# Optimization experiments

Measured on AMD Instinct MI355X. Metric: run time of the kernel, lower is better.

The kernel has to match this reference:

```python
import jax, jax.numpy as jnp
import numpy as np

B, C, H, W = 256, 3, 84, 84
HID, VOCAB = 768, 50257
INPUT_DIM = H * W
EPS = 1e-8


def setup_inputs() -> dict:
    key = jax.random.key(0)
    k1, k2, k3 = jax.random.split(key, 3)
    observations = jax.random.normal(k1, (B, C, H, W), dtype=jnp.float32)
    word_embs = jax.random.normal(k2, (VOCAB, HID), dtype=jnp.float32)
    # torch.normal(mean=0, std=1/sqrt(hidden_dim), size=(hidden_dim, input_dim))
    rand_obs_proj = jax.random.normal(k3, (HID, INPUT_DIM), dtype=jnp.float32) / np.sqrt(HID)
    return {"observations": observations, "word_embs": word_embs,
            "rand_obs_proj": rand_obs_proj, "beta": 8}


def reference(observations, word_embs, rand_obs_proj, beta):
    # _preprocess_obs: mean over channel dim, then flatten each sample
    obs = observations.mean(axis=1).reshape(observations.shape[0], -1)  # [B, H*W]
    q = obs @ rand_obs_proj.T                                           # [B, HID]
    q_norm = jnp.linalg.norm(q, axis=-1, keepdims=True)                 # [B, 1]
    e_norm = jnp.linalg.norm(word_embs, axis=-1)[None, :]               # [1, V]
    sims = (q @ word_embs.T) / (q_norm * e_norm + EPS)                  # [B, V]
    softm = jax.nn.softmax(beta * sims, axis=-1)
    state = softm @ word_embs                                           # [B, HID]
    return state
```

## Files before the change

### kernel.cpp

```cpp
#include <hip/hip_runtime.h>


#define VOCAB 50257
#define VPAD  50304
#define HID   768
#define BATCH 256
#define IN    7056
#define INPAD 7072
#define NPAIR (INPAD / 2)
#define SPLITS 32
#define CHUNK 1600
#define QSPLITS 17
#define QCHUNK 416

typedef __attribute__((ext_vector_type(8))) __bf16 bf16x8;
typedef __attribute__((ext_vector_type(4))) float f32x4;

__device__ inline unsigned short f2bf(float f) {
  union { float f; unsigned u; } v; v.f = f;
  unsigned r = v.u + 0x7fffu + ((v.u >> 16) & 1u);
  return (unsigned short)(r >> 16);
}
__device__ inline unsigned pack2(float lo, float hi) {
  return (unsigned)f2bf(lo) | ((unsigned)f2bf(hi) << 16);
}

__global__ __launch_bounds__(256, 3) void k_wprep(const float* __restrict__ W,
                                                  unsigned* __restrict__ Wb,
                                                  unsigned* __restrict__ WbT,
                                                  float* __restrict__ inv_en) {
  __shared__ unsigned short Sb[32][772];
  __shared__ float ssb[32][8];
  const int t = threadIdx.x;
  const int lane = t & 63, wave = t >> 6;
  const int v0 = blockIdx.x * 32;

  float4 xv[8][3];
#pragma unroll
  for (int rr = 0; rr < 8; rr++) {
    const int v = v0 + wave * 8 + rr;
    const int vc = (v < VOCAB) ? v : (VOCAB - 1);
    const float* wrow = &W[(size_t)vc * HID + lane * 4];
#pragma unroll
    for (int c = 0; c < 3; c++)
      xv[rr][c] = *(const float4*)(wrow + c * 256);
  }
#pragma unroll
  for (int rr = 0; rr < 8; rr++) {
    const int row = wave * 8 + rr;
    const int v = v0 + row;
    const bool valid = (v < VOCAB);
    unsigned* wbrow = &Wb[(size_t)v * (HID / 2) + lane * 2];
    float ss = 0.f;
#pragma unroll
    for (int c = 0; c < 3; c++) {
      float4 x = xv[rr][c];
      if (!valid) x = (float4){0.f, 0.f, 0.f, 0.f};
      unsigned lo = pack2(x.x, x.y), hi = pack2(x.z, x.w);
      *(uint2*)&Sb[row][c * 256 + lane * 4] = (uint2){lo, hi};
      *(uint2*)&wbrow[c * 128] = (uint2){lo, hi};
      ss += x.x * x.x + x.y * x.y + x.z * x.z + x.w * x.w;
    }
    ss += __shfl_xor(ss, 1, 64);
    ss += __shfl_xor(ss, 2, 64);
    ss += __shfl_xor(ss, 4, 64);
    if ((lane & 7) == 0) ssb[row][lane >> 3] = ss;
  }
  __syncthreads();
  {
    const int row = t >> 3, j = t & 7;
    float s = ssb[row][j];
    s += __shfl_xor(s, 1, 64);
    s += __shfl_xor(s, 2, 64);
    s += __shfl_xor(s, 4, 64);
    if (j == 0) {
      const int v = v0 + row;
      inv_en[v] = (v < VOCAB) ? (1.f / sqrtf(s)) : 0.f;
    }
  }
  for (int p = 0; p < 12; p++) {
    int hr = p * 64 + (t >> 2), li = t & 3;
    unsigned u[4];
    for (int j = 0; j < 4; j++) {
      int vl = li * 8 + j * 2;
      u[j] = (unsigned)Sb[vl][hr] | ((unsigned)Sb[vl + 1][hr] << 16);
    }
    *(uint4*)&WbT[(size_t)hr * (VPAD / 2) + (v0 >> 1) + li * 4] = *(const uint4*)u;
  }
}

__global__ __launch_bounds__(256) void k_obs(const float* __restrict__ obs,
                                             unsigned* __restrict__ obsb) {
  int b = blockIdx.x, t = threadIdx.x;
  const size_t base = (size_t)b * 3 * IN;
  for (int p = t; p < NPAIR; p += 256) {
    float x = 0.f, y = 0.f;
    if (2 * p < IN) {
      float2 a0 = *(const float2*)&obs[base + 2 * p];
      float2 a1 = *(const float2*)&obs[base + IN + 2 * p];
      float2 a2 = *(const float2*)&obs[base + 2 * IN + 2 * p];
      x = (a0.x + a1.x + a2.x) * (1.f / 3.f);
      y = (a0.y + a1.y + a2.y) * (1.f / 3.f);
    }
    obsb[b * NPAIR + p] = pack2(x, y);
  }
}

__global__ __launch_bounds__(256) void k_proj(const float* __restrict__ proj,
                                              unsigned* __restrict__ projb) {
  int h = blockIdx.x, t = threadIdx.x;
  for (int p = t; p < NPAIR; p += 256) {
    float x = 0.f, y = 0.f;
    if (2 * p < IN) {
      float2 xy = *(const float2*)&proj[(size_t)h * IN + 2 * p];
      x = xy.x; y = xy.y;
    }
    projb[h * NPAIR + p] = pack2(x, y);
  }
}


__global__ __launch_bounds__(256) void k_qgemm(const unsigned short* __restrict__ A,
                                               const unsigned short* __restrict__ Bm,
                                               float* __restrict__ qp) {
  __shared__ unsigned short As[64][32];
  __shared__ unsigned short Bs[64][32];
  const int t = threadIdx.x;
  const int lane = t & 63, wave = t >> 6;
  const int wm = wave >> 1, wn = wave & 1;
  const int quad = lane >> 4, lo = lane & 15;
  const int m0 = blockIdx.y * 64, n0 = blockIdx.x * 64;
  const int split = blockIdx.z;
  const int kbeg = split * QCHUNK, kend = kbeg + QCHUNK;
  const int ar = t >> 2, ac = (t & 3) * 8;
  f32x4 acc[2][2];
  for (int i = 0; i < 2; i++)
    for (int j = 0; j < 2; j++) acc[i][j] = (f32x4){0.f, 0.f, 0.f, 0.f};
  const unsigned short* aptr = &A[(m0 + ar) * INPAD + ac];
  const unsigned short* bptr = &Bm[(n0 + ar) * INPAD + ac];
  for (int k0 = kbeg; k0 < kend; k0 += 32) {
    uint4 av = *(const uint4*)(aptr + k0);
    uint4 bv = *(const uint4*)(bptr + k0);
    __syncthreads();
    *(uint4*)&As[ar][ac] = av;
    *(uint4*)&Bs[ar][ac] = bv;
    __syncthreads();
    bf16x8 af[2], bfr[2];
    for (int i = 0; i < 2; i++) {
      af[i]  = *(const bf16x8*)&As[wm * 32 + i * 16 + lo][quad * 8];
      bfr[i] = *(const bf16x8*)&Bs[wn * 32 + i * 16 + lo][quad * 8];
    }
    for (int mi = 0; mi < 2; mi++)
      for (int ni = 0; ni < 2; ni++)
        acc[mi][ni] = __builtin_amdgcn_mfma_f32_16x16x32_bf16(af[mi], bfr[ni], acc[mi][ni], 0, 0, 0);
  }
  float* outp = qp + (size_t)split * BATCH * HID;
  for (int mi = 0; mi < 2; mi++)
    for (int ni = 0; ni < 2; ni++)
      for (int r = 0; r < 4; r++) {
        int row = m0 + wm * 32 + mi * 16 + quad * 4 + r;
        int col = n0 + wn * 32 + ni * 16 + lo;
        outp[row * HID + col] = acc[mi][ni][r];
      }
}

__global__ __launch_bounds__(384) void k_qhat(const float* __restrict__ qp,
                                              const int* __restrict__ beta,
                                              unsigned* __restrict__ qhat,
                                              float* __restrict__ l) {
  int b = blockIdx.x, t = threadIdx.x;
  float x = 0.f, y = 0.f;
  for (int s = 0; s < QSPLITS; s++) {
    float2 p = *(const float2*)&qp[(size_t)s * BATCH * HID + b * HID + 2 * t];
    x += p.x; y += p.y;
  }
  float ss = x * x + y * y;
  for (int m = 1; m < 64; m <<= 1) ss += __shfl_xor(ss, m, 64);
  __shared__ float sacc[6];
  if ((t & 63) == 0) sacc[t >> 6] = ss;
  __syncthreads();
  float tot = sacc[0] + sacc[1] + sacc[2] + sacc[3] + sacc[4] + sacc[5];
  float scale = (float)beta[0] / sqrtf(tot);
  qhat[b * (HID / 2) + t] = pack2(x * scale, y * scale);
  if (t == 0) l[b] = 0.f;
}


__global__ __launch_bounds__(256) void k_gemm1(const unsigned short* __restrict__ A,
                                               const unsigned short* __restrict__ Bm,
                                               const float* __restrict__ inv_en,
                                               unsigned short* __restrict__ E,
                                               float* __restrict__ l) {
  __shared__ unsigned short As[128][32];
  __shared__ unsigned short Bs[128][32];
  __shared__ unsigned short Et[128][128];
  __shared__ float rowsum[128];
  const int t = threadIdx.x;
  const int lane = t & 63, wave = t >> 6;
  const int wm = wave >> 1, wn = wave & 1;
  const int quad = lane >> 4, lo = lane & 15;
  const int m0 = blockIdx.x * 128, n0 = blockIdx.y * 128;
  const int ar = t >> 2, ac = (t & 3) * 8;
  if (t < 128) rowsum[t] = 0.f;
  f32x4 acc[4][4];
  for (int i = 0; i < 4; i++)
    for (int j = 0; j < 4; j++) acc[i][j] = (f32x4){0.f, 0.f, 0.f, 0.f};
  const unsigned short* aptr  = &A[(m0 + ar) * HID + ac];
  const unsigned short* aptr2 = &A[(m0 + ar + 64) * HID + ac];
  const unsigned short* bptr  = &Bm[(size_t)(n0 + ar) * HID + ac];
  const unsigned short* bptr2 = &Bm[(size_t)(n0 + ar + 64) * HID + ac];
  for (int k0 = 0; k0 < HID; k0 += 32) {
    uint4 av0 = *(const uint4*)(aptr + k0);
    uint4 av1 = *(const uint4*)(aptr2 + k0);
    uint4 bv0 = *(const uint4*)(bptr + k0);
    uint4 bv1 = *(const uint4*)(bptr2 + k0);
    __syncthreads();
    *(uint4*)&As[ar][ac]      = av0;
    *(uint4*)&As[ar + 64][ac] = av1;
    *(uint4*)&Bs[ar][ac]      = bv0;
    *(uint4*)&Bs[ar + 64][ac] = bv1;
    __syncthreads();
    bf16x8 af[4], bfr[4];
    for (int i = 0; i < 4; i++) {
      af[i]  = *(const bf16x8*)&As[wm * 64 + i * 16 + lo][quad * 8];
      bfr[i] = *(const bf16x8*)&Bs[wn * 64 + i * 16 + lo][quad * 8];
    }
    for (int mi = 0; mi < 4; mi++)
      for (int ni = 0; ni < 4; ni++)
        acc[mi][ni] = __builtin_amdgcn_mfma_f32_16x16x32_bf16(af[mi], bfr[ni], acc[mi][ni], 0, 0, 0);
  }
  for (int mi = 0; mi < 4; mi++)
    for (int ni = 0; ni < 4; ni++) {
      int cl = wn * 64 + ni * 16 + lo;
      int vg = n0 + cl;
      bool valid = (vg < VOCAB);
      float ie = inv_en[vg];
      for (int r = 0; r < 4; r++) {
        int row = wm * 64 + mi * 16 + quad * 4 + r;
        float e = valid ? __expf(acc[mi][ni][r] * ie) : 0.f;
        Et[row][cl] = f2bf(e);
        float s = e;
        s += __shfl_xor(s, 1, 64);
        s += __shfl_xor(s, 2, 64);
        s += __shfl_xor(s, 4, 64);
        s += __shfl_xor(s, 8, 64);
        if (lo == 0) atomicAdd(&rowsum[row], s);
      }
    }
  __syncthreads();
  for (int i = 0; i < 8; i++) {
    int idx = t + i * 256;
    int row = idx >> 4, j = idx & 15;
    *(uint4*)&E[(size_t)(m0 + row) * VPAD + n0 + j * 8] = *(const uint4*)&Et[row][j * 8];
  }
  if (t < 128) atomicAdd(&l[m0 + t], rowsum[t]);
}


__global__ __launch_bounds__(256) void k_gemm2(const unsigned short* __restrict__ A,
                                               const unsigned short* __restrict__ Bm,
                                               float* __restrict__ Pp) {
  __shared__ unsigned short As[128][32];
  __shared__ unsigned short Bs[128][32];
  const int t = threadIdx.x;
  const int lane = t & 63, wave = t >> 6;
  const int wm = wave >> 1, wn = wave & 1;
  const int quad = lane >> 4, lo = lane & 15;
  const int m0 = blockIdx.x * 128, n0 = blockIdx.y * 128;
  const int split = blockIdx.z;
  const int kbeg = split * CHUNK;
  const int kend = (kbeg + CHUNK < VPAD) ? kbeg + CHUNK : VPAD;
  const int ar = t >> 2, ac = (t & 3) * 8;
  f32x4 acc[4][4];
  for (int i = 0; i < 4; i++)
    for (int j = 0; j < 4; j++) acc[i][j] = (f32x4){0.f, 0.f, 0.f, 0.f};
  const unsigned short* aptr  = &A[(size_t)(m0 + ar) * VPAD + ac];
  const unsigned short* aptr2 = &A[(size_t)(m0 + ar + 64) * VPAD + ac];
  const unsigned short* bptr  = &Bm[(size_t)(n0 + ar) * VPAD + ac];
  const unsigned short* bptr2 = &Bm[(size_t)(n0 + ar + 64) * VPAD + ac];
  for (int k0 = kbeg; k0 < kend; k0 += 32) {
    uint4 av0 = *(const uint4*)(aptr + k0);
    uint4 av1 = *(const uint4*)(aptr2 + k0);
    uint4 bv0 = *(const uint4*)(bptr + k0);
    uint4 bv1 = *(const uint4*)(bptr2 + k0);
    __syncthreads();
    *(uint4*)&As[ar][ac]      = av0;
    *(uint4*)&As[ar + 64][ac] = av1;
    *(uint4*)&Bs[ar][ac]      = bv0;
    *(uint4*)&Bs[ar + 64][ac] = bv1;
    __syncthreads();
    bf16x8 af[4], bfr[4];
    for (int i = 0; i < 4; i++) {
      af[i]  = *(const bf16x8*)&As[wm * 64 + i * 16 + lo][quad * 8];
      bfr[i] = *(const bf16x8*)&Bs[wn * 64 + i * 16 + lo][quad * 8];
    }
    for (int mi = 0; mi < 4; mi++)
      for (int ni = 0; ni < 4; ni++)
        acc[mi][ni] = __builtin_amdgcn_mfma_f32_16x16x32_bf16(af[mi], bfr[ni], acc[mi][ni], 0, 0, 0);
  }
  float* outp = Pp + (size_t)split * HID * BATCH;
  for (int mi = 0; mi < 4; mi++)
    for (int ni = 0; ni < 4; ni++)
      for (int r = 0; r < 4; r++) {
        int h = m0 + wm * 64 + mi * 16 + quad * 4 + r;
        int b = n0 + wn * 64 + ni * 16 + lo;
        outp[h * BATCH + b] = acc[mi][ni][r];
      }
}

__global__ __launch_bounds__(256) void k_reduce(const float* __restrict__ Pp,
                                                const float* __restrict__ l,
                                                float* __restrict__ out) {
  int idx = blockIdx.x * 256 + threadIdx.x;
  int h = idx >> 8, b = idx & 255;
  float s = 0.f;
  for (int i = 0; i < SPLITS; i++) s += Pp[(size_t)i * (HID * BATCH) + idx];
  out[b * HID + h] = s / l[b];
}


extern "C" void kernel_launch(void* const* d_in, const int* in_sizes, int n_in,
                              void* d_out, int out_size, void* d_ws, size_t ws_size,
                              hipStream_t stream) {
  const float* obs  = (const float*)d_in[0];
  const float* W    = (const float*)d_in[1];
  const float* proj = (const float*)d_in[2];
  const int* beta   = (const int*)d_in[3];
  float* out = (float*)d_out;

  char* ws = (char*)d_ws;
  size_t off = 0;
  auto alloc = [&](size_t bytes) -> void* {
    void* p = ws + off;
    off = (off + bytes + 255) & ~(size_t)255;
    return p;
  };
  unsigned short* Wb    = (unsigned short*)alloc((size_t)VPAD * HID * 2);
  unsigned short* WbT   = (unsigned short*)alloc((size_t)HID * VPAD * 2);
  float* inv_en         = (float*)alloc((size_t)VPAD * 4);
  unsigned short* obsb  = (unsigned short*)alloc((size_t)BATCH * INPAD * 2);
  unsigned short* projb = (unsigned short*)alloc((size_t)HID * INPAD * 2);
  unsigned short* qhat  = (unsigned short*)alloc((size_t)BATCH * HID * 2);
  float* l              = (float*)alloc((size_t)BATCH * 4);
  unsigned short* E     = (unsigned short*)alloc((size_t)BATCH * VPAD * 2);
  float* Pp             = (float*)alloc((size_t)SPLITS * BATCH * HID * 4);
  float* qp             = Pp;
  (void)ws_size; (void)in_sizes; (void)n_in; (void)out_size;

  k_wprep<<<dim3(VPAD / 32), dim3(256), 0, stream>>>(W, (unsigned*)Wb, (unsigned*)WbT, inv_en);
  k_obs  <<<dim3(BATCH), dim3(256), 0, stream>>>(obs, (unsigned*)obsb);
  k_proj <<<dim3(HID), dim3(256), 0, stream>>>(proj, (unsigned*)projb);
  k_qgemm<<<dim3(HID / 64, BATCH / 64, QSPLITS), dim3(256), 0, stream>>>(obsb, projb, qp);
  k_qhat <<<dim3(BATCH), dim3(384), 0, stream>>>(qp, beta, (unsigned*)qhat, l);
  k_gemm1<<<dim3(BATCH / 128, VPAD / 128), dim3(256), 0, stream>>>(qhat, Wb, inv_en, E, l);
  k_gemm2<<<dim3(HID / 128, BATCH / 128, SPLITS), dim3(256), 0, stream>>>(WbT, E, Pp);
  k_reduce<<<dim3(BATCH * HID / 256), dim3(256), 0, stream>>>(Pp, l, out);
}
```

Measured before the change: 449.1 us.

## Drop transposed W copy; transpose Wb tiles in LDS inside gemm2

```diff
diff --git a/kernel.cpp b/kernel.cpp
--- a/kernel.cpp
+++ b/kernel.cpp
@@ -27,9 +27,7 @@
 
 __global__ __launch_bounds__(256, 3) void k_wprep(const float* __restrict__ W,
                                                   unsigned* __restrict__ Wb,
-                                                  unsigned* __restrict__ WbT,
                                                   float* __restrict__ inv_en) {
-  __shared__ unsigned short Sb[32][772];
   __shared__ float ssb[32][8];
   const int t = threadIdx.x;
   const int lane = t & 63, wave = t >> 6;
@@ -45,6 +43,7 @@
     for (int c = 0; c < 3; c++)
       xv[rr][c] = *(const float4*)(wrow + c * 256);
   }
+  __builtin_amdgcn_sched_barrier(0);
 #pragma unroll
   for (int rr = 0; rr < 8; rr++) {
     const int row = wave * 8 + rr;
@@ -56,9 +55,7 @@
     for (int c = 0; c < 3; c++) {
       float4 x = xv[rr][c];
       if (!valid) x = (float4){0.f, 0.f, 0.f, 0.f};
-      unsigned lo = pack2(x.x, x.y), hi = pack2(x.z, x.w);
-      *(uint2*)&Sb[row][c * 256 + lane * 4] = (uint2){lo, hi};
-      *(uint2*)&wbrow[c * 128] = (uint2){lo, hi};
+      *(uint2*)&wbrow[c * 128] = (uint2){pack2(x.x, x.y), pack2(x.z, x.w)};
       ss += x.x * x.x + x.y * x.y + x.z * x.z + x.w * x.w;
     }
     ss += __shfl_xor(ss, 1, 64);
@@ -77,15 +74,6 @@
       const int v = v0 + row;
       inv_en[v] = (v < VOCAB) ? (1.f / sqrtf(s)) : 0.f;
     }
-  }
-  for (int p = 0; p < 12; p++) {
-    int hr = p * 64 + (t >> 2), li = t & 3;
-    unsigned u[4];
-    for (int j = 0; j < 4; j++) {
-      int vl = li * 8 + j * 2;
-      u[j] = (unsigned)Sb[vl][hr] | ((unsigned)Sb[vl + 1][hr] << 16);
-    }
-    *(uint4*)&WbT[(size_t)hr * (VPAD / 2) + (v0 >> 1) + li * 4] = *(const uint4*)u;
   }
 }
 
@@ -257,10 +245,10 @@
 }
 
 
-__global__ __launch_bounds__(256) void k_gemm2(const unsigned short* __restrict__ A,
+__global__ __launch_bounds__(256) void k_gemm2(const unsigned short* __restrict__ Wb,
                                                const unsigned short* __restrict__ Bm,
                                                float* __restrict__ Pp) {
-  __shared__ unsigned short As[128][32];
+  __shared__ unsigned short As[128][34];
   __shared__ unsigned short Bs[128][32];
   const int t = threadIdx.x;
   const int lane = t & 63, wave = t >> 6;
@@ -270,28 +258,37 @@
   const int split = blockIdx.z;
   const int kbeg = split * CHUNK;
   const int kend = (kbeg + CHUNK < VPAD) ? kbeg + CHUNK : VPAD;
+  const int sv = t >> 3, shc = t & 7;
   const int ar = t >> 2, ac = (t & 3) * 8;
   f32x4 acc[4][4];
   for (int i = 0; i < 4; i++)
     for (int j = 0; j < 4; j++) acc[i][j] = (f32x4){0.f, 0.f, 0.f, 0.f};
-  const unsigned short* aptr  = &A[(size_t)(m0 + ar) * VPAD + ac];
-  const unsigned short* aptr2 = &A[(size_t)(m0 + ar + 64) * VPAD + ac];
   const unsigned short* bptr  = &Bm[(size_t)(n0 + ar) * VPAD + ac];
   const unsigned short* bptr2 = &Bm[(size_t)(n0 + ar + 64) * VPAD + ac];
   for (int k0 = kbeg; k0 < kend; k0 += 32) {
-    uint4 av0 = *(const uint4*)(aptr + k0);
-    uint4 av1 = *(const uint4*)(aptr2 + k0);
+    uint4 a0  = *(const uint4*)&Wb[(size_t)(k0 + sv) * HID + m0 + shc * 8];
+    uint4 a1  = *(const uint4*)&Wb[(size_t)(k0 + sv) * HID + m0 + (shc + 8) * 8];
     uint4 bv0 = *(const uint4*)(bptr + k0);
     uint4 bv1 = *(const uint4*)(bptr2 + k0);
     __syncthreads();
-    *(uint4*)&As[ar][ac]      = av0;
-    *(uint4*)&As[ar + 64][ac] = av1;
+    {
+      const unsigned short* e0 = (const unsigned short*)&a0;
+      const unsigned short* e1 = (const unsigned short*)&a1;
+#pragma unroll
+      for (int j = 0; j < 8; j++) {
+        As[shc * 8 + j][sv]       = e0[j];
+        As[(shc + 8) * 8 + j][sv] = e1[j];
+      }
+    }
     *(uint4*)&Bs[ar][ac]      = bv0;
     *(uint4*)&Bs[ar + 64][ac] = bv1;
     __syncthreads();
     bf16x8 af[4], bfr[4];
+#pragma unroll
     for (int i = 0; i < 4; i++) {
-      af[i]  = *(const bf16x8*)&As[wm * 64 + i * 16 + lo][quad * 8];
+      const unsigned* rp = (const unsigned*)&As[wm * 64 + i * 16 + lo][quad * 8];
+      uint4 u; u.x = rp[0]; u.y = rp[1]; u.z = rp[2]; u.w = rp[3];
+      af[i]  = *(const bf16x8*)&u;
       bfr[i] = *(const bf16x8*)&Bs[wn * 64 + i * 16 + lo][quad * 8];
     }
     for (int mi = 0; mi < 4; mi++)
@@ -336,7 +333,6 @@
     return p;
   };
   unsigned short* Wb    = (unsigned short*)alloc((size_t)VPAD * HID * 2);
-  unsigned short* WbT   = (unsigned short*)alloc((size_t)HID * VPAD * 2);
   float* inv_en         = (float*)alloc((size_t)VPAD * 4);
   unsigned short* obsb  = (unsigned short*)alloc((size_t)BATCH * INPAD * 2);
   unsigned short* projb = (unsigned short*)alloc((size_t)HID * INPAD * 2);
@@ -347,12 +343,12 @@
   float* qp             = Pp;
   (void)ws_size; (void)in_sizes; (void)n_in; (void)out_size;
 
-  k_wprep<<<dim3(VPAD / 32), dim3(256), 0, stream>>>(W, (unsigned*)Wb, (unsigned*)WbT, inv_en);
+  k_wprep<<<dim3(VPAD / 32), dim3(256), 0, stream>>>(W, (unsigned*)Wb, inv_en);
   k_obs  <<<dim3(BATCH), dim3(256), 0, stream>>>(obs, (unsigned*)obsb);
   k_proj <<<dim3(HID), dim3(256), 0, stream>>>(proj, (unsigned*)projb);
   k_qgemm<<<dim3(HID / 64, BATCH / 64, QSPLITS), dim3(256), 0, stream>>>(obsb, projb, qp);
   k_qhat <<<dim3(BATCH), dim3(384), 0, stream>>>(qp, beta, (unsigned*)qhat, l);
   k_gemm1<<<dim3(BATCH / 128, VPAD / 128), dim3(256), 0, stream>>>(qhat, Wb, inv_en, E, l);
-  k_gemm2<<<dim3(HID / 128, BATCH / 128, SPLITS), dim3(256), 0, stream>>>(WbT, E, Pp);
+  k_gemm2<<<dim3(HID / 128, BATCH / 128, SPLITS), dim3(256), 0, stream>>>(Wb, E, Pp);
   k_reduce<<<dim3(BATCH * HID / 256), dim3(256), 0, stream>>>(Pp, l, out);
 }
```

Result: faster. 415.0 us (-7.6%).
